# Kernel optimization log

Hardware: AMD Instinct MI355X
Metric: run time of the kernel (lower is better)

## Reference

```python
import jax, jax.numpy as jnp
import numpy as np

B, S, E, H = 4, 1024, 1024, 16
D = E // H
LN_EPS = 1e-5
W_SCALE = 0.02  # keep pre-softmax scores positive and moderate


def _linear(x, W, b):
    return x @ W + b


def _layernorm(x, g, b):
    m = jnp.mean(x, axis=-1, keepdims=True)
    v = jnp.mean((x - m) ** 2, axis=-1, keepdims=True)
    return (x - m) * jax.lax.rsqrt(v + LN_EPS) * g + b


def setup_inputs() -> dict:
    key = jax.random.key(0)
    ks = jax.random.split(key, 24)
    u = lambda k, shape, s=1.0: jax.random.uniform(k, shape, dtype=jnp.float32) * s
    inp = {
        'value': u(ks[0], (B, S, E)),
        'key':   u(ks[1], (B, S, E)),
        'query': u(ks[2], (B, S, E)),
        'mask':  jnp.ones((B, 1, 1, S), dtype=jnp.int32),
        # attention projections (W stored as [in, out])
        'Wv': u(ks[3], (E, E), W_SCALE), 'bv': u(ks[4], (E,), W_SCALE),
        'Wk': u(ks[5], (E, E), W_SCALE), 'bk': u(ks[6], (E,), W_SCALE),
        'Wq': u(ks[7], (E, E), W_SCALE), 'bq': u(ks[8], (E,), W_SCALE),
        'Wo': u(ks[9], (E, E), W_SCALE), 'bo': u(ks[10], (E,), W_SCALE),
        # feed-forward
        'W1': u(ks[11], (E, 4 * E), W_SCALE), 'b1': u(ks[12], (4 * E,), W_SCALE),
        'W2': u(ks[13], (4 * E, E), W_SCALE), 'b2': u(ks[14], (E,), W_SCALE),
        # layer norms
        'g1': jnp.ones((E,), jnp.float32), 'be1': jnp.zeros((E,), jnp.float32),
        'g2': jnp.ones((E,), jnp.float32), 'be2': jnp.zeros((E,), jnp.float32),
    }
    return inp


def reference(value, key, query, mask, Wv, bv, Wk, bk, Wq, bq, Wo, bo,
              W1, b1, W2, b2, g1, be1, g2, be2):
    b, q_len, _ = query.shape
    v = _linear(value, Wv, bv).reshape(b, -1, H, D)   # [B,K,H,D]
    k = _linear(key, Wk, bk).reshape(b, -1, H, D)     # [B,K,H,D]
    q = _linear(query, Wq, bq).reshape(b, q_len, H, D)
    att = jnp.einsum('bqhd,bkhd->bhqk', q, k)         # raw scores
    att = jnp.where(mask == 0, -jnp.inf, att)
    att = jnp.power(att, -0.5)                        # custom score^{-1/2} transform
    att = jax.nn.softmax(att, axis=3)
    ctx = jnp.einsum('bhqk,bkhd->bqhd', att, v).reshape(b, q_len, E)
    attn_out = _linear(ctx, Wo, bo)
    x = _layernorm(attn_out + query, g1, be1)         # dropout = identity (eval)
    ff = _linear(jax.nn.relu(_linear(x, W1, b1)), W2, b2)
    return _layernorm(ff + x, g2, be2)
```

## Files before the change

kernel.cpp:

```cpp
#include <hip/hip_runtime.h>
#include <hip/hip_bf16.h>
#include <cstdint>

typedef __hip_bfloat16 bf16;
typedef float f32x4 __attribute__((ext_vector_type(4)));
typedef short bf16x8 __attribute__((ext_vector_type(8)));
typedef short bf16x4v __attribute__((ext_vector_type(4)));

#define S_LEN 1024
#define EDIM  1024

__device__ __forceinline__ float bfs2f(short s) {
  return __uint_as_float(((unsigned)(unsigned short)s) << 16);
}
__device__ __forceinline__ short f2bfs(float f) {
  union { __hip_bfloat16 h; short s; } u;
  u.h = __float2bfloat16(f);
  return u.s;
}
__device__ __forceinline__ void glds16(const void* g, void* l) {
  __builtin_amdgcn_global_load_lds(
      (const __attribute__((address_space(1))) void*)g,
      (__attribute__((address_space(3))) void*)l, 16, 0, 0);
}
__device__ __forceinline__ float score_xform(float s) {
  float r, e;
  asm("v_rsq_f32 %0, %1" : "=v"(r) : "v"(s));
  r *= 1.44269504088896f;
  asm("v_exp_f32 %0, %1" : "=v"(e) : "v"(r));
  return e;
}
__device__ __forceinline__ int xcd_swz(int bid, int nwg) {
  const int q = nwg >> 3, r = nwg & 7, xcd = bid & 7, j = bid >> 3;
  return (xcd < r ? xcd * (q + 1) : r * (q + 1) + (xcd - r) * q) + j;
}
#define BAR() do { __builtin_amdgcn_s_barrier(); asm volatile("" ::: "memory"); } while (0)
#define WAITV(n) asm volatile("s_waitcnt vmcnt(" #n ")" ::: "memory")

struct Cvt3 { const float* in[3]; bf16* out[3]; };
__global__ __launch_bounds__(256)
void k_cvt3(Cvt3 p, int n4) {
  const float4* in = (const float4*)p.in[blockIdx.y];
  bf16x4v* out = (bf16x4v*)p.out[blockIdx.y];
  for (int i = blockIdx.x * 256 + threadIdx.x; i < n4; i += gridDim.x * 256) {
    float4 v = in[i];
    bf16x4v o;
    o[0] = f2bfs(v.x); o[1] = f2bfs(v.y); o[2] = f2bfs(v.z); o[3] = f2bfs(v.w);
    out[i] = o;
  }
}

struct TAll { const float* in[6]; bf16* out[6]; };
__global__ void k_transpose_all(TAll p) {
  int t = blockIdx.x;
  int z, tr, tc, R, C;
  if (t < 4096)      { z = t >> 10; R = 1024; C = 1024; int i = t & 1023; tr = i >> 5; tc = i & 31; }
  else if (t < 8192) { z = 4; R = 1024; C = 4096; int i = t - 4096; tr = i >> 7; tc = i & 127; }
  else               { z = 5; R = 4096; C = 1024; int i = t - 8192; tr = i >> 5; tc = i & 31; }
  __shared__ bf16 tile[32][33];
  const float* in = p.in[z];
  bf16* out = p.out[z];
  const int c0 = tc * 32, r0 = tr * 32;
  const int x = threadIdx.x;
  for (int yy = threadIdx.y; yy < 32; yy += 8)
    tile[yy][x] = __float2bfloat16(in[(size_t)(r0 + yy) * C + c0 + x]);
  __syncthreads();
  for (int yy = threadIdx.y; yy < 32; yy += 8)
    out[(size_t)(c0 + yy) * R + r0 + x] = tile[x][yy];
}

__global__ void k_transpose_v(const bf16* __restrict__ v, bf16* __restrict__ vt) {
  __shared__ bf16 t[32][33];
  const int bh = blockIdx.z;
  const bf16* in = v + (size_t)(bh >> 4) * S_LEN * EDIM + (bh & 15) * 64;
  bf16* out = vt + (size_t)bh * 64 * S_LEN;
  const int d0 = blockIdx.x * 32, s0 = blockIdx.y * 32;
  const int x = threadIdx.x;
  for (int yy = threadIdx.y; yy < 32; yy += 8)
    t[yy][x] = in[(size_t)(s0 + yy) * EDIM + d0 + x];
  __syncthreads();
  for (int yy = threadIdx.y; yy < 32; yy += 8)
    out[(size_t)(d0 + yy) * S_LEN + s0 + x] = t[x][yy];
}

template <int RELU, int OUT_F32, int HAS_BIAS>
__device__ __forceinline__ void gemm8_body(
    const bf16* __restrict__ A, int lda, const bf16* __restrict__ Bt, int ldb,
    const float* __restrict__ bias, void* __restrict__ Cout, int ldc,
    int K, int koff, int bm, int bn, char* smem) {
  const int tid = threadIdx.x, lane = tid & 63, wid = tid >> 6;
  const int wm = wid >> 2;
  const int wn = wid & 3;
  const int fr = lane & 15, fg = lane >> 4;
  const int sw = (fr & 7) << 4;

  const int rr = lane >> 3;
  const int cc = ((lane & 7) ^ rr) << 3;

  #define STG(src, ld, dstoff)                                                  \
    {                                                                           \
      const bf16* _s = (src);                                                   \
      _Pragma("unroll")                                                         \
      for (int _j = 0; _j < 2; _j++) {                                          \
        const int _L = wid * 2 + _j;                                            \
        glds16(_s + (size_t)(_L * 8 + rr) * (ld) + cc, smem + (dstoff) + _L * 1024); \
      }                                                                         \
    }

  const bf16* Abase = A + (size_t)bm * lda + koff;
  const bf16* Bbase = Bt + (size_t)bn * ldb + koff;
  const int nt = K >> 6;

  STG(Abase, lda, 0);
  STG(Abase + (size_t)128 * lda, lda, 16384);
  STG(Bbase, ldb, 32768);
  STG(Bbase + (size_t)128 * ldb, ldb, 49152);
  if (nt > 1) {
    STG(Bbase + 64, ldb, 65536 + 32768);
    STG(Bbase + (size_t)128 * ldb + 64, ldb, 65536 + 49152);
  }
  WAITV(0);
  BAR();

  f32x4 acc[8][4] = {};
  bf16x8 af[8][2], bf[4][2];

  const int aRd = wm * 16384 + fr * 128;
  const int bRd = 32768 + (wn >> 1) * 16384 + (wn & 1) * 8192 + fr * 128;
  const int c0s = (0 * 64 + fg * 16) ^ sw;
  const int c1s = (1 * 64 + fg * 16) ^ sw;

  for (int n = 0; n < nt; n++) {
    const int buf = (n & 1) << 16;
    const int nbuf = buf ^ 65536;
    const char* sb = smem + buf;
    const int kA = (n + 1) << 6;
    const int kB = (n + 2) << 6;

#pragma unroll
    for (int j = 0; j < 4; j++) {
      bf[j][0] = *(const bf16x8*)(sb + bRd + j * 2048 + c0s);
      bf[j][1] = *(const bf16x8*)(sb + bRd + j * 2048 + c1s);
    }
#pragma unroll
    for (int i = 0; i < 8; i++) {
      af[i][0] = *(const bf16x8*)(sb + aRd + i * 2048 + c0s);
      af[i][1] = *(const bf16x8*)(sb + aRd + i * 2048 + c1s);
    }
    if (n + 1 < nt) {
      STG(Abase + kA, lda, nbuf);
      STG(Abase + (size_t)128 * lda + kA, lda, nbuf + 16384);
    }
    BAR();
    __builtin_amdgcn_s_setprio(1);
#pragma unroll
    for (int i = 0; i < 4; i++)
#pragma unroll
      for (int j = 0; j < 4; j++) {
        acc[i][j] = __builtin_amdgcn_mfma_f32_16x16x32_bf16(af[i][0], bf[j][0], acc[i][j], 0, 0, 0);
        acc[i][j] = __builtin_amdgcn_mfma_f32_16x16x32_bf16(af[i][1], bf[j][1], acc[i][j], 0, 0, 0);
      }
    __builtin_amdgcn_s_setprio(0);

    if (n + 2 < nt) {
      STG(Bbase + kB, ldb, buf + 32768);
      STG(Bbase + (size_t)128 * ldb + kB, ldb, buf + 49152);
    }
    __builtin_amdgcn_s_setprio(1);
#pragma unroll
    for (int i = 0; i < 4; i++)
#pragma unroll
      for (int j = 0; j < 4; j++) {
        acc[i + 4][j] = __builtin_amdgcn_mfma_f32_16x16x32_bf16(af[i + 4][0], bf[j][0], acc[i + 4][j], 0, 0, 0);
        acc[i + 4][j] = __builtin_amdgcn_mfma_f32_16x16x32_bf16(af[i + 4][1], bf[j][1], acc[i + 4][j], 0, 0, 0);
      }
    __builtin_amdgcn_s_setprio(0);
    if (n + 2 < nt) { WAITV(4); } else { WAITV(0); }
    BAR();
  }
  #undef STG

  float bv4[4];
#pragma unroll
  for (int j = 0; j < 4; j++)
    bv4[j] = HAS_BIAS ? bias[bn + wn * 64 + j * 16 + fr] : 0.f;
#pragma unroll
  for (int i = 0; i < 8; i++) {
    const size_t rowb = (size_t)bm + wm * 128 + i * 16 + fg * 4;
#pragma unroll
    for (int r = 0; r < 4; r++) {
#pragma unroll
      for (int j = 0; j < 4; j++) {
        float v = acc[i][j][r] + bv4[j];
        if (RELU) v = fmaxf(v, 0.f);
        const size_t idx = (rowb + r) * (size_t)ldc + bn + wn * 64 + j * 16 + fr;
        if (OUT_F32) ((float*)Cout)[idx] = v;
        else ((bf16*)Cout)[idx] = __float2bfloat16(v);
      }
    }
  }
}

struct G8Args {
  const bf16* A; int lda; const bf16* Bt; int ldb; const float* bias;
  void* C[4]; int ldc; int koffz[4]; int Kzz[4];
};
template <int RELU, int OUT_F32, int HAS_BIAS>
__global__ __launch_bounds__(512, 2)
void k_gemm8(G8Args a) {
  __shared__ __align__(16) char smem[131072];
  const int nwg = gridDim.x * gridDim.y;
  const int bid = xcd_swz(blockIdx.y * gridDim.x + blockIdx.x, nwg);
  const int bx = bid % gridDim.x, by = bid / gridDim.x;
  const int z = blockIdx.z;
  gemm8_body<RELU, OUT_F32, HAS_BIAS>(
      a.A, a.lda, a.Bt, a.ldb, a.bias, a.C[z], a.ldc,
      a.Kzz[z], a.koffz[z], by * 256, bx * 256, smem);
}

struct QkvArgs { const bf16* A[3]; const bf16* B[3]; const float* bias[3]; bf16* C[3]; };
__global__ __launch_bounds__(512, 2)
void k_gemm8_qkv(QkvArgs p) {
  __shared__ __align__(16) char smem[131072];
  const int nwg = gridDim.x * gridDim.y;
  const int bid = xcd_swz(blockIdx.y * gridDim.x + blockIdx.x, nwg);
  const int bx = bid % (int)gridDim.x;
  int by = bid / (int)gridDim.x;
  const int grp = by >> 4;
  by &= 15;
  gemm8_body<0, 0, 1>(p.A[grp], 1024, p.B[grp], 1024, p.bias[grp],
                      (void*)p.C[grp], 1024, 1024, 0, by * 256, bx * 256, smem);
}

__global__ __launch_bounds__(256)
void k_attn(const bf16* __restrict__ q, const bf16* __restrict__ k,
            const bf16* __restrict__ vt, bf16* __restrict__ ctx) {
  const int bh = blockIdx.x;
  const int qt = blockIdx.y;
  const int b = bh >> 4, h = bh & 15;
  const int tid = threadIdx.x, lane = tid & 63, w = tid >> 6;
  const int fr = lane & 15, fg = lane >> 4;
  const bf16* Q  = q  + (size_t)b * S_LEN * EDIM + h * 64;
  const bf16* Kp = k  + (size_t)b * S_LEN * EDIM + h * 64;
  const bf16* V  = vt + (size_t)bh * 64 * S_LEN;

  __shared__ __align__(16) bf16 lK[2][64 * 64];
  __shared__ __align__(16) bf16 lV[2][64 * 64];
  __shared__ __align__(16) bf16 eL[4][32][72];

  const int srow = lane >> 3;
  const int scol = (((lane & 7) ^ srow) << 3);
  const int rsw  = (fr & 7) << 3;

  bf16x8 qf[2][2];
#pragma unroll
  for (int i = 0; i < 2; i++)
#pragma unroll
    for (int ks = 0; ks < 2; ks++)
      qf[i][ks] = *(const bf16x8*)(Q + (size_t)(qt * 128 + w * 32 + i * 16 + fr) * EDIM + ks * 32 + fg * 8);

#pragma unroll
  for (int c = 0; c < 2; c++) {
    const int r = w * 8 + c * 32 + srow;
    glds16(Kp + (size_t)r * EDIM + scol, (char*)&lK[0][(w * 8 + c * 32) * 64]);
    glds16(V + (size_t)r * S_LEN + scol, (char*)&lV[0][(w * 8 + c * 32) * 64]);
  }
  __syncthreads();

  f32x4 accO[2][4] = {};
  float lsum[2][4] = {};
  int cur = 0;
  for (int kt = 0; kt < S_LEN; kt += 64) {
    if (kt + 64 < S_LEN) {
#pragma unroll
      for (int c = 0; c < 2; c++) {
        const int r = w * 8 + c * 32 + srow;
        glds16(Kp + (size_t)(kt + 64 + r) * EDIM + scol,
               (char*)&lK[cur ^ 1][(w * 8 + c * 32) * 64]);
        glds16(V + (size_t)r * S_LEN + kt + 64 + scol,
               (char*)&lV[cur ^ 1][(w * 8 + c * 32) * 64]);
      }
    }
    f32x4 accS[2][4] = {};
#pragma unroll
    for (int ks = 0; ks < 2; ks++)
#pragma unroll
      for (int j = 0; j < 4; j++) {
        bf16x8 kf = *(const bf16x8*)(&lK[cur][(j * 16 + fr) * 64 + ((ks * 32 + fg * 8) ^ rsw)]);
#pragma unroll
        for (int i = 0; i < 2; i++)
          accS[i][j] = __builtin_amdgcn_mfma_f32_16x16x32_bf16(qf[i][ks], kf, accS[i][j], 0, 0, 0);
      }
#pragma unroll
    for (int i = 0; i < 2; i++)
#pragma unroll
      for (int j = 0; j < 4; j++)
#pragma unroll
        for (int r = 0; r < 4; r++) {
          float p = score_xform(accS[i][j][r]);
          lsum[i][r] += p;
          eL[w][i * 16 + fg * 4 + r][j * 16 + fr] = __float2bfloat16(p);
        }
#pragma unroll
    for (int ks = 0; ks < 2; ks++) {
      bf16x8 af[2];
#pragma unroll
      for (int i = 0; i < 2; i++)
        af[i] = *(const bf16x8*)(&eL[w][i * 16 + fr][ks * 32 + fg * 8]);
#pragma unroll
      for (int j = 0; j < 4; j++) {
        bf16x8 vf = *(const bf16x8*)(&lV[cur][(j * 16 + fr) * 64 + ((ks * 32 + fg * 8) ^ rsw)]);
#pragma unroll
        for (int i = 0; i < 2; i++)
          accO[i][j] = __builtin_amdgcn_mfma_f32_16x16x32_bf16(af[i], vf, accO[i][j], 0, 0, 0);
      }
    }
    __syncthreads();
    cur ^= 1;
  }

#pragma unroll
  for (int i = 0; i < 2; i++)
#pragma unroll
    for (int r = 0; r < 4; r++) {
      float s = lsum[i][r];
      s += __shfl_xor(s, 1, 64);
      s += __shfl_xor(s, 2, 64);
      s += __shfl_xor(s, 4, 64);
      s += __shfl_xor(s, 8, 64);
      lsum[i][r] = s;
    }
#pragma unroll
  for (int i = 0; i < 2; i++)
#pragma unroll
    for (int r = 0; r < 4; r++) {
      const size_t qrow = (size_t)qt * 128 + w * 32 + i * 16 + fg * 4 + r;
      const float inv = 1.0f / lsum[i][r];
#pragma unroll
      for (int j = 0; j < 4; j++)
        ctx[((size_t)b * S_LEN + qrow) * EDIM + h * 64 + j * 16 + fr] =
            __float2bfloat16(accO[i][j][r] * inv);
    }
}

struct LnP { const float* p[4]; };
template <int NP, int RES_F32, int OUT_F32>
__global__ __launch_bounds__(256)
void k_ln_resN(LnP pp, const float* __restrict__ bias, const void* res_,
               const float* __restrict__ g, const float* __restrict__ be,
               void* out_) {
  const int row = blockIdx.x;
  const int tid = threadIdx.x;
  const int lane = tid & 63, wid = tid >> 6;
  const size_t base = (size_t)row * EDIM + tid * 4;
  float4 c = *(const float4*)(bias + tid * 4);
  float x[4] = {c.x, c.y, c.z, c.w};
#pragma unroll
  for (int t = 0; t < NP; t++) {
    float4 v = *(const float4*)(pp.p[t] + base);
    x[0] += v.x; x[1] += v.y; x[2] += v.z; x[3] += v.w;
  }
  if (RES_F32) {
    float4 v = *(const float4*)((const float*)res_ + base);
    x[0] += v.x; x[1] += v.y; x[2] += v.z; x[3] += v.w;
  } else {
    bf16x4v v = *(const bf16x4v*)((const bf16*)res_ + base);
#pragma unroll
    for (int i = 0; i < 4; i++) x[i] += bfs2f(v[i]);
  }

  float s = x[0] + x[1] + x[2] + x[3];
#pragma unroll
  for (int o = 32; o >= 1; o >>= 1) s += __shfl_xor(s, o, 64);
  __shared__ float red[4], red2[4];
  if (lane == 0) red[wid] = s;
  __syncthreads();
  const float mean = (red[0] + red[1] + red[2] + red[3]) * (1.0f / 1024.0f);

  float d[4], s2 = 0.f;
#pragma unroll
  for (int i = 0; i < 4; i++) { d[i] = x[i] - mean; s2 += d[i] * d[i]; }
#pragma unroll
  for (int o = 32; o >= 1; o >>= 1) s2 += __shfl_xor(s2, o, 64);
  if (lane == 0) red2[wid] = s2;
  __syncthreads();
  const float var = (red2[0] + red2[1] + red2[2] + red2[3]) * (1.0f / 1024.0f);
  const float inv = rsqrtf(var + 1e-5f);

  float4 g4 = *(const float4*)(g + tid * 4);
  float4 b4 = *(const float4*)(be + tid * 4);
  float o0 = d[0] * inv * g4.x + b4.x;
  float o1 = d[1] * inv * g4.y + b4.y;
  float o2 = d[2] * inv * g4.z + b4.z;
  float o3 = d[3] * inv * g4.w + b4.w;
  if (OUT_F32) {
    *(float4*)((float*)out_ + base) = make_float4(o0, o1, o2, o3);
  } else {
    bf16x4v o;
    o[0] = f2bfs(o0); o[1] = f2bfs(o1); o[2] = f2bfs(o2); o[3] = f2bfs(o3);
    *(bf16x4v*)((bf16*)out_ + base) = o;
  }
}

extern "C" void kernel_launch(void* const* d_in, const int* in_sizes, int n_in,
                              void* d_out, int out_size, void* d_ws, size_t ws_size,
                              hipStream_t stream) {
  const float* value = (const float*)d_in[0];
  const float* key_  = (const float*)d_in[1];
  const float* query = (const float*)d_in[2];
  const float* Wv = (const float*)d_in[4];  const float* bv = (const float*)d_in[5];
  const float* Wk = (const float*)d_in[6];  const float* bk = (const float*)d_in[7];
  const float* Wq = (const float*)d_in[8];  const float* bq = (const float*)d_in[9];
  const float* Wo = (const float*)d_in[10]; const float* bo = (const float*)d_in[11];
  const float* W1 = (const float*)d_in[12]; const float* b1 = (const float*)d_in[13];
  const float* W2 = (const float*)d_in[14]; const float* b2 = (const float*)d_in[15];
  const float* g1 = (const float*)d_in[16]; const float* be1 = (const float*)d_in[17];
  const float* g2 = (const float*)d_in[18]; const float* be2 = (const float*)d_in[19];

  char* wsb = (char*)d_ws;
  const size_t MB = 1024 * 1024;
  bf16* W1T = (bf16*)(wsb + 0 * MB);
  bf16* W2T = (bf16*)(wsb + 8 * MB);
  bf16* WqT = (bf16*)(wsb + 16 * MB);
  bf16* WkT = (bf16*)(wsb + 18 * MB);
  bf16* WvT = (bf16*)(wsb + 20 * MB);
  bf16* WoT = (bf16*)(wsb + 22 * MB);
  bf16* qx  = (bf16*)(wsb + 24 * MB);
  bf16* kx  = (bf16*)(wsb + 32 * MB);
  bf16* vx  = (bf16*)(wsb + 40 * MB);
  bf16* qb  = (bf16*)(wsb + 48 * MB);
  bf16* kb  = (bf16*)(wsb + 56 * MB);
  bf16* vb  = (bf16*)(wsb + 64 * MB);
  bf16* vtb = (bf16*)(wsb + 72 * MB);
  bf16* ctx = (bf16*)(wsb + 24 * MB);
  float* p0w = (float*)(wsb + 32 * MB);
  float* p1w = (float*)(wsb + 48 * MB);
  float* p2w = (float*)(wsb + 64 * MB);
  bf16* xb  = (bf16*)(wsb + 16 * MB);
  bf16* h1  = (bf16*)(wsb + 24 * MB);
  float* f1 = (float*)(wsb + 56 * MB);
  float* f2 = (float*)(wsb + 72 * MB);
  float* f3 = (float*)(wsb + 88 * MB);
  const int splitF = (ws_size >= 104 * MB) ? 4 : (ws_size >= 88 * MB) ? 3 : 2;

  const dim3 tb(32, 8);
  Cvt3 cp;
  cp.in[0] = query; cp.out[0] = qx;
  cp.in[1] = key_;  cp.out[1] = kx;
  cp.in[2] = value; cp.out[2] = vx;
  k_cvt3<<<dim3(1024, 3), 256, 0, stream>>>(cp, 1024 * 1024);

  TAll ta;
  ta.in[0] = Wq; ta.out[0] = WqT;
  ta.in[1] = Wk; ta.out[1] = WkT;
  ta.in[2] = Wv; ta.out[2] = WvT;
  ta.in[3] = Wo; ta.out[3] = WoT;
  ta.in[4] = W1; ta.out[4] = W1T;
  ta.in[5] = W2; ta.out[5] = W2T;
  k_transpose_all<<<12288, tb, 0, stream>>>(ta);

  QkvArgs qp;
  qp.A[0] = qx; qp.B[0] = WqT; qp.bias[0] = bq; qp.C[0] = qb;
  qp.A[1] = kx; qp.B[1] = WkT; qp.bias[1] = bk; qp.C[1] = kb;
  qp.A[2] = vx; qp.B[2] = WvT; qp.bias[2] = bv; qp.C[2] = vb;
  k_gemm8_qkv<<<dim3(4, 48), 512, 0, stream>>>(qp);

  k_transpose_v<<<dim3(2, 32, 64), tb, 0, stream>>>(vb, vtb);
  k_attn<<<dim3(64, 8), 256, 0, stream>>>(qb, kb, vtb, ctx);

  G8Args wo;
  wo.A = ctx; wo.lda = 1024; wo.Bt = WoT; wo.ldb = 1024; wo.bias = nullptr;
  wo.C[0] = p0w; wo.C[1] = p1w; wo.C[2] = p2w; wo.C[3] = nullptr;
  wo.ldc = 1024;
  wo.koffz[0] = 0;   wo.Kzz[0] = 384;
  wo.koffz[1] = 384; wo.Kzz[1] = 320;
  wo.koffz[2] = 704; wo.Kzz[2] = 320;
  wo.koffz[3] = 0;   wo.Kzz[3] = 64;
  k_gemm8<0, 1, 0><<<dim3(4, 16, 3), 512, 0, stream>>>(wo);
  LnP l1; l1.p[0] = p0w; l1.p[1] = p1w; l1.p[2] = p2w; l1.p[3] = nullptr;
  k_ln_resN<3, 1, 0><<<4096, 256, 0, stream>>>(l1, bo, query, g1, be1, xb);

  G8Args ff1;
  ff1.A = xb; ff1.lda = 1024; ff1.Bt = W1T; ff1.ldb = 1024; ff1.bias = b1;
  ff1.C[0] = h1; ff1.C[1] = nullptr; ff1.C[2] = nullptr; ff1.C[3] = nullptr;
  ff1.ldc = 4096;
  ff1.koffz[0] = 0; ff1.Kzz[0] = 1024;
  ff1.koffz[1] = 0; ff1.Kzz[1] = 64;
  ff1.koffz[2] = 0; ff1.Kzz[2] = 64;
  ff1.koffz[3] = 0; ff1.Kzz[3] = 64;
  k_gemm8<1, 0, 1><<<dim3(16, 16, 1), 512, 0, stream>>>(ff1);

  G8Args ff2;
  ff2.A = h1; ff2.lda = 4096; ff2.Bt = W2T; ff2.ldb = 4096; ff2.bias = nullptr;
  ff2.C[0] = d_out; ff2.C[1] = f1; ff2.C[2] = f2; ff2.C[3] = f3;
  ff2.ldc = 1024;
  if (splitF == 4) {
    for (int z = 0; z < 4; z++) { ff2.koffz[z] = z * 1024; ff2.Kzz[z] = 1024; }
  } else if (splitF == 3) {
    ff2.koffz[0] = 0;    ff2.Kzz[0] = 1344;
    ff2.koffz[1] = 1344; ff2.Kzz[1] = 1344;
    ff2.koffz[2] = 2688; ff2.Kzz[2] = 1408;
    ff2.koffz[3] = 0;    ff2.Kzz[3] = 64;
  } else {
    ff2.koffz[0] = 0;    ff2.Kzz[0] = 2048;
    ff2.koffz[1] = 2048; ff2.Kzz[1] = 2048;
    ff2.koffz[2] = 0;    ff2.Kzz[2] = 64;
    ff2.koffz[3] = 0;    ff2.Kzz[3] = 64;
  }
  k_gemm8<0, 1, 0><<<dim3(4, 16, splitF), 512, 0, stream>>>(ff2);

  LnP l2;
  l2.p[0] = (const float*)d_out; l2.p[1] = f1; l2.p[2] = f2; l2.p[3] = f3;
  if (splitF == 4)
    k_ln_resN<4, 0, 1><<<4096, 256, 0, stream>>>(l2, b2, xb, g2, be2, (float*)d_out);
  else if (splitF == 3)
    k_ln_resN<3, 0, 1><<<4096, 256, 0, stream>>>(l2, b2, xb, g2, be2, (float*)d_out);
  else
    k_ln_resN<2, 0, 1><<<4096, 256, 0, stream>>>(l2, b2, xb, g2, be2, (float*)d_out);
}
```

Baseline: 223.6 us.

## Triple-buffer GEMM A tiles with deeper prefetch and fuse prep kernels

The GEMM main loop now prefetches both A and B tiles two K-steps ahead. A uses a three-slot LDS ring and B a two-slot ring, which grows shared memory to 160 KB and loosens the vmcnt waits. The intent is to hide more global-load latency behind the MFMA work. Separately, the fp32-to-bf16 activation conversion is folded into the weight transpose/convert kernel, saving one launch. The larger LDS footprint allows at most one workgroup per CU and adds more index bookkeeping in the loop.

```diff
diff --git a/kernel.cpp b/kernel.cpp
--- a/kernel.cpp
+++ b/kernel.cpp
@@ -37,36 +37,39 @@
 #define BAR() do { __builtin_amdgcn_s_barrier(); asm volatile("" ::: "memory"); } while (0)
 #define WAITV(n) asm volatile("s_waitcnt vmcnt(" #n ")" ::: "memory")
 
-struct Cvt3 { const float* in[3]; bf16* out[3]; };
-__global__ __launch_bounds__(256)
-void k_cvt3(Cvt3 p, int n4) {
-  const float4* in = (const float4*)p.in[blockIdx.y];
-  bf16x4v* out = (bf16x4v*)p.out[blockIdx.y];
-  for (int i = blockIdx.x * 256 + threadIdx.x; i < n4; i += gridDim.x * 256) {
-    float4 v = in[i];
-    bf16x4v o;
-    o[0] = f2bfs(v.x); o[1] = f2bfs(v.y); o[2] = f2bfs(v.z); o[3] = f2bfs(v.w);
-    out[i] = o;
-  }
-}
-
-struct TAll { const float* in[6]; bf16* out[6]; };
-__global__ void k_transpose_all(TAll p) {
-  int t = blockIdx.x;
-  int z, tr, tc, R, C;
-  if (t < 4096)      { z = t >> 10; R = 1024; C = 1024; int i = t & 1023; tr = i >> 5; tc = i & 31; }
-  else if (t < 8192) { z = 4; R = 1024; C = 4096; int i = t - 4096; tr = i >> 7; tc = i & 127; }
-  else               { z = 5; R = 4096; C = 1024; int i = t - 8192; tr = i >> 5; tc = i & 31; }
-  __shared__ bf16 tile[32][33];
-  const float* in = p.in[z];
-  bf16* out = p.out[z];
-  const int c0 = tc * 32, r0 = tr * 32;
-  const int x = threadIdx.x;
-  for (int yy = threadIdx.y; yy < 32; yy += 8)
-    tile[yy][x] = __float2bfloat16(in[(size_t)(r0 + yy) * C + c0 + x]);
-  __syncthreads();
-  for (int yy = threadIdx.y; yy < 32; yy += 8)
-    out[(size_t)(c0 + yy) * R + r0 + x] = tile[x][yy];
+struct Prep { const float* win[6]; bf16* wout[6]; const float* ain[3]; bf16* aout[3]; };
+__global__ void k_prep(Prep p) {
+  const int t = blockIdx.x;
+  if (t < 12288) {
+    int z, tr, tc, R, C;
+    if (t < 4096)      { z = t >> 10; R = 1024; C = 1024; int i = t & 1023; tr = i >> 5; tc = i & 31; }
+    else if (t < 8192) { z = 4; R = 1024; C = 4096; int i = t - 4096; tr = i >> 7; tc = i & 127; }
+    else               { z = 5; R = 4096; C = 1024; int i = t - 8192; tr = i >> 5; tc = i & 31; }
+    __shared__ bf16 tile[32][33];
+    const float* in = p.win[z];
+    bf16* out = p.wout[z];
+    const int c0 = tc * 32, r0 = tr * 32;
+    const int x = threadIdx.x;
+    for (int yy = threadIdx.y; yy < 32; yy += 8)
+      tile[yy][x] = __float2bfloat16(in[(size_t)(r0 + yy) * C + c0 + x]);
+    __syncthreads();
+    for (int yy = threadIdx.y; yy < 32; yy += 8)
+      out[(size_t)(c0 + yy) * R + r0 + x] = tile[x][yy];
+  } else {
+    const int idx = t - 12288;
+    const int z = idx >> 10, chunk = idx & 1023;
+    const int tid = threadIdx.y * 32 + threadIdx.x;
+    const float4* in = (const float4*)p.ain[z];
+    bf16x4v* out = (bf16x4v*)p.aout[z];
+#pragma unroll
+    for (int s = 0; s < 4; s++) {
+      const int i = chunk * 256 + s * 262144 + tid;
+      float4 v = in[i];
+      bf16x4v o;
+      o[0] = f2bfs(v.x); o[1] = f2bfs(v.y); o[2] = f2bfs(v.z); o[3] = f2bfs(v.w);
+      out[i] = o;
+    }
+  }
 }
 
 __global__ void k_transpose_v(const bf16* __restrict__ v, bf16* __restrict__ vt) {
@@ -113,43 +116,44 @@
 
   STG(Abase, lda, 0);
   STG(Abase + (size_t)128 * lda, lda, 16384);
-  STG(Bbase, ldb, 32768);
-  STG(Bbase + (size_t)128 * ldb, ldb, 49152);
-  if (nt > 1) {
-    STG(Bbase + 64, ldb, 65536 + 32768);
-    STG(Bbase + (size_t)128 * ldb + 64, ldb, 65536 + 49152);
-  }
-  WAITV(0);
+  STG(Bbase, ldb, 98304);
+  STG(Bbase + (size_t)128 * ldb, ldb, 98304 + 16384);
+  STG(Abase + 64, lda, 32768);
+  STG(Abase + (size_t)128 * lda + 64, lda, 32768 + 16384);
+  STG(Bbase + 64, ldb, 131072);
+  STG(Bbase + (size_t)128 * ldb + 64, ldb, 131072 + 16384);
+  WAITV(8);
   BAR();
 
   f32x4 acc[8][4] = {};
-  bf16x8 af[8][2], bf[4][2];
+  bf16x8 af[8][2], bfr[4][2];
 
   const int aRd = wm * 16384 + fr * 128;
-  const int bRd = 32768 + (wn >> 1) * 16384 + (wn & 1) * 8192 + fr * 128;
-  const int c0s = (0 * 64 + fg * 16) ^ sw;
-  const int c1s = (1 * 64 + fg * 16) ^ sw;
-
+  const int bRd = (wn >> 1) * 16384 + (wn & 1) * 8192 + fr * 128;
+  const int c0s = (fg * 16) ^ sw;
+  const int c1s = (64 + fg * 16) ^ sw;
+
+  int sa = 0, sb = 0;
   for (int n = 0; n < nt; n++) {
-    const int buf = (n & 1) << 16;
-    const int nbuf = buf ^ 65536;
-    const char* sb = smem + buf;
-    const int kA = (n + 1) << 6;
-    const int kB = (n + 2) << 6;
+    const char* pa = smem + sa * 32768;
+    const char* pb = smem + 98304 + sb * 32768;
+    const int kn = (n + 2) << 6;
+    const bool st = (n + 2) < nt;
+    const int sa2 = (sa >= 1) ? sa - 1 : 2;
 
 #pragma unroll
     for (int j = 0; j < 4; j++) {
-      bf[j][0] = *(const bf16x8*)(sb + bRd + j * 2048 + c0s);
-      bf[j][1] = *(const bf16x8*)(sb + bRd + j * 2048 + c1s);
+      bfr[j][0] = *(const bf16x8*)(pb + bRd + j * 2048 + c0s);
+      bfr[j][1] = *(const bf16x8*)(pb + bRd + j * 2048 + c1s);
     }
 #pragma unroll
     for (int i = 0; i < 8; i++) {
-      af[i][0] = *(const bf16x8*)(sb + aRd + i * 2048 + c0s);
-      af[i][1] = *(const bf16x8*)(sb + aRd + i * 2048 + c1s);
-    }
-    if (n + 1 < nt) {
-      STG(Abase + kA, lda, nbuf);
-      STG(Abase + (size_t)128 * lda + kA, lda, nbuf + 16384);
+      af[i][0] = *(const bf16x8*)(pa + aRd + i * 2048 + c0s);
+      af[i][1] = *(const bf16x8*)(pa + aRd + i * 2048 + c1s);
+    }
+    if (st) {
+      STG(Abase + kn, lda, sa2 * 32768);
+      STG(Abase + (size_t)128 * lda + kn, lda, sa2 * 32768 + 16384);
     }
     BAR();
     __builtin_amdgcn_s_setprio(1);
@@ -157,26 +161,28 @@
     for (int i = 0; i < 4; i++)
 #pragma unroll
       for (int j = 0; j < 4; j++) {
-        acc[i][j] = __builtin_amdgcn_mfma_f32_16x16x32_bf16(af[i][0], bf[j][0], acc[i][j], 0, 0, 0);
-        acc[i][j] = __builtin_amdgcn_mfma_f32_16x16x32_bf16(af[i][1], bf[j][1], acc[i][j], 0, 0, 0);
+        acc[i][j] = __builtin_amdgcn_mfma_f32_16x16x32_bf16(af[i][0], bfr[j][0], acc[i][j], 0, 0, 0);
+        acc[i][j] = __builtin_amdgcn_mfma_f32_16x16x32_bf16(af[i][1], bfr[j][1], acc[i][j], 0, 0, 0);
       }
     __builtin_amdgcn_s_setprio(0);
 
-    if (n + 2 < nt) {
-      STG(Bbase + kB, ldb, buf + 32768);
-      STG(Bbase + (size_t)128 * ldb + kB, ldb, buf + 49152);
+    if (st) {
+      STG(Bbase + kn, ldb, 98304 + sb * 32768);
+      STG(Bbase + (size_t)128 * ldb + kn, ldb, 98304 + sb * 32768 + 16384);
     }
     __builtin_amdgcn_s_setprio(1);
 #pragma unroll
     for (int i = 0; i < 4; i++)
 #pragma unroll
       for (int j = 0; j < 4; j++) {
-        acc[i + 4][j] = __builtin_amdgcn_mfma_f32_16x16x32_bf16(af[i + 4][0], bf[j][0], acc[i + 4][j], 0, 0, 0);
-        acc[i + 4][j] = __builtin_amdgcn_mfma_f32_16x16x32_bf16(af[i + 4][1], bf[j][1], acc[i + 4][j], 0, 0, 0);
+        acc[i + 4][j] = __builtin_amdgcn_mfma_f32_16x16x32_bf16(af[i + 4][0], bfr[j][0], acc[i + 4][j], 0, 0, 0);
+        acc[i + 4][j] = __builtin_amdgcn_mfma_f32_16x16x32_bf16(af[i + 4][1], bfr[j][1], acc[i + 4][j], 0, 0, 0);
       }
     __builtin_amdgcn_s_setprio(0);
-    if (n + 2 < nt) { WAITV(4); } else { WAITV(0); }
+    if (st) { WAITV(8); } else { WAITV(0); }
     BAR();
+    sa = (sa == 2) ? 0 : sa + 1;
+    sb ^= 1;
   }
   #undef STG
 
@@ -208,7 +214,7 @@
 template <int RELU, int OUT_F32, int HAS_BIAS>
 __global__ __launch_bounds__(512, 2)
 void k_gemm8(G8Args a) {
-  __shared__ __align__(16) char smem[131072];
+  __shared__ __align__(16) char smem[163840];
   const int nwg = gridDim.x * gridDim.y;
   const int bid = xcd_swz(blockIdx.y * gridDim.x + blockIdx.x, nwg);
   const int bx = bid % gridDim.x, by = bid / gridDim.x;
@@ -221,7 +227,7 @@
 struct QkvArgs { const bf16* A[3]; const bf16* B[3]; const float* bias[3]; bf16* C[3]; };
 __global__ __launch_bounds__(512, 2)
 void k_gemm8_qkv(QkvArgs p) {
-  __shared__ __align__(16) char smem[131072];
+  __shared__ __align__(16) char smem[163840];
   const int nwg = gridDim.x * gridDim.y;
   const int bid = xcd_swz(blockIdx.y * gridDim.x + blockIdx.x, nwg);
   const int bx = bid % (int)gridDim.x;
@@ -444,20 +450,17 @@
   const int splitF = (ws_size >= 104 * MB) ? 4 : (ws_size >= 88 * MB) ? 3 : 2;
 
   const dim3 tb(32, 8);
-  Cvt3 cp;
-  cp.in[0] = query; cp.out[0] = qx;
-  cp.in[1] = key_;  cp.out[1] = kx;
-  cp.in[2] = value; cp.out[2] = vx;
-  k_cvt3<<<dim3(1024, 3), 256, 0, stream>>>(cp, 1024 * 1024);
-
-  TAll ta;
-  ta.in[0] = Wq; ta.out[0] = WqT;
-  ta.in[1] = Wk; ta.out[1] = WkT;
-  ta.in[2] = Wv; ta.out[2] = WvT;
-  ta.in[3] = Wo; ta.out[3] = WoT;
-  ta.in[4] = W1; ta.out[4] = W1T;
-  ta.in[5] = W2; ta.out[5] = W2T;
-  k_transpose_all<<<12288, tb, 0, stream>>>(ta);
+  Prep pp;
+  pp.win[0] = Wq; pp.wout[0] = WqT;
+  pp.win[1] = Wk; pp.wout[1] = WkT;
+  pp.win[2] = Wv; pp.wout[2] = WvT;
+  pp.win[3] = Wo; pp.wout[3] = WoT;
+  pp.win[4] = W1; pp.wout[4] = W1T;
+  pp.win[5] = W2; pp.wout[5] = W2T;
+  pp.ain[0] = query; pp.aout[0] = qx;
+  pp.ain[1] = key_;  pp.aout[1] = kx;
+  pp.ain[2] = value; pp.aout[2] = vx;
+  k_prep<<<15360, tb, 0, stream>>>(pp);
 
   QkvArgs qp;
   qp.A[0] = qx; qp.B[0] = WqT; qp.bias[0] = bq; qp.C[0] = qb;
```

New measurement: 221.1 us. About the same (-1.1%).
